# Optimization experiments

Hardware: AMD Instinct MI355X
Metric: run time of the kernel (lower is better)

Reference implementation:

```python
import jax, jax.numpy as jnp
import numpy as np
from jax import lax

K_ADA = 0.1
EPS = 1e-5
B, G = 2, 96
C0, C1, C2, C3, F = 1, 16, 32, 64, 64


def adanorm(x, g):
    # AdaNorm over the last (channel) axis: w * (1 - k*xn) * xn
    mean = x.mean(-1, keepdims=True)
    var = ((x - mean) ** 2).mean(-1, keepdims=True) + EPS
    xn = (x - mean) * lax.rsqrt(var)
    return g * (1.0 - K_ADA * xn) * xn


def conv3d(x, w, b, stride):
    # x: [B,D,H,W,Cin], w: [3,3,3,Cin,Cout], padding 1
    y = lax.conv_general_dilated(x, w, (stride,) * 3, [(1, 1)] * 3,
                                 dimension_numbers=('NDHWC', 'DHWIO', 'NDHWC'))
    return y + b


def downsample_mask(m):
    # active output sites of SparseConv3d(k=3, s=2, p=1): any active input in window
    return lax.reduce_window(m, 0.0, lax.max, (1, 3, 3, 3), (1, 2, 2, 2),
                             [(0, 0), (1, 1), (1, 1), (1, 1)])


def setup_inputs() -> dict:
    key = jax.random.key(0)
    ks = jax.random.split(key, 20)
    mask = (jax.random.uniform(ks[0], (B, G, G, G)) < 0.05).astype(jnp.float32)
    x = jax.random.normal(ks[1], (B, G, G, G, C0), jnp.float32) * mask[..., None]

    def wconv(k, cin, cout):
        return jax.random.normal(k, (3, 3, 3, cin, cout), jnp.float32) / np.sqrt(27.0 * cin)

    inp = {'x': x, 'mask': mask}
    chans = [(C0, C1), (C1, C2), (C2, C2), (C2, C3), (C3, C3)]
    for i, (ci, co) in enumerate(chans, start=1):
        inp[f'w{i}'] = wconv(ks[2 * i], ci, co)
        inp[f'b{i}'] = jax.random.normal(ks[2 * i + 1], (co,), jnp.float32) * 0.01
        inp[f'g{i}'] = jnp.ones((co,), jnp.float32)
    inp['wh'] = jax.random.normal(ks[12], (C3, F), jnp.float32) / np.sqrt(C3)
    inp['bh'] = jax.random.normal(ks[13], (F,), jnp.float32) * 0.01
    inp['gh'] = jnp.ones((F,), jnp.float32)
    return inp


def reference(x, mask, w1, b1, g1, w2, b2, g2, w3, b3, g3, w4, b4, g4, w5, b5, g5, wh, bh, gh):
    m1 = mask
    h = conv3d(x, w1, b1, 1) * m1[..., None]            # SubMConv3d
    h = jax.nn.relu(adanorm(h, g1)) * m1[..., None]
    m2 = downsample_mask(m1)
    h = conv3d(h, w2, b2, 2) * m2[..., None]            # SparseConv3d s=2
    h = jax.nn.relu(adanorm(h, g2)) * m2[..., None]
    h = conv3d(h, w3, b3, 1) * m2[..., None]            # SubMConv3d
    h = jax.nn.relu(adanorm(h, g3)) * m2[..., None]
    m3 = downsample_mask(m2)
    h = conv3d(h, w4, b4, 2) * m3[..., None]            # SparseConv3d s=2
    h = jax.nn.relu(adanorm(h, g4)) * m3[..., None]
    h = conv3d(h, w5, b5, 1) * m3[..., None]            # SubMConv3d
    h = jax.nn.relu(adanorm(h, g5)) * m3[..., None]
    # SparseGlobalMaxPool over active voxels
    neg = jnp.asarray(-3.0e38, h.dtype)
    pooled = jnp.where(m3[..., None] > 0, h, neg).max(axis=(1, 2, 3))  # [B, C3]
    # head: Linear -> AdaNorm -> ReLU -> Dropout(eval = identity)
    out = jax.nn.relu(adanorm(pooled @ wh + bh, gh))
    return out
```

## Files before the change

kernel.cpp:

```cpp
#include <hip/hip_runtime.h>
#include <math.h>

#define K_ADA 0.1f
#define NEPS 1e-5f

typedef __attribute__((ext_vector_type(8))) short short8;
typedef __attribute__((ext_vector_type(4))) float f32x4;
typedef unsigned short ushort_t;

__device__ __forceinline__ ushort_t f2b(float f) {
    union { float f; unsigned u; } v; v.f = f;
    unsigned r = (v.u + 0x7fffu + ((v.u >> 16) & 1u)) >> 16;
    return (ushort_t)r;
}

__device__ __forceinline__ float wave_sum64(float v) {
#pragma unroll
    for (int m = 1; m < 64; m <<= 1) v += __shfl_xor(v, m, 64);
    return v;
}

__host__ __device__ constexpr int tapd2(int tap) {
    return tap >= 27 ? 0 : (tap / 9) * 81 + ((tap / 3) % 3) * 9 + (tap % 3);
}

template <int CIN, int COUT>
__device__ __forceinline__ void pack_w_el(const float* __restrict__ w,
                                          ushort_t* __restrict__ wp, int t)
{
    constexpr int NKH = CIN / 32;
    constexpr int NCT = COUT / 16;
    int jj = t & 7;
    int lane = (t >> 3) & 63;
    int rest = t >> 9;
    int kh = rest % NKH;
    int rest2 = rest / NKH;
    int ct = rest2 % NCT;
    int tap = rest2 / NCT;
    int cin = kh * 32 + (lane >> 4) * 8 + jj;
    int cout = ct * 16 + (lane & 15);
    wp[t] = f2b(w[(tap * CIN + cin) * COUT + cout]);
}

__global__ __launch_bounds__(256) void prep_k(
    const float* __restrict__ w1, const float* __restrict__ w2,
    const float* __restrict__ w3, const float* __restrict__ w4,
    const float* __restrict__ w5, const float* __restrict__ m1,
    ushort_t* __restrict__ wp1, ushort_t* __restrict__ wp2,
    ushort_t* __restrict__ wp3, ushort_t* __restrict__ wp4,
    ushort_t* __restrict__ wp5, float* __restrict__ m2,
    float* __restrict__ zeropad, int* __restrict__ counters,
    float* __restrict__ pooled)
{
    int t = blockIdx.x * 256 + threadIdx.x;
    if (t < 512) {
        int jj = t & 7;
        int lane = t >> 3;
        int tap = (lane >> 4) * 8 + jj;
        int cout = lane & 15;
        wp1[t] = (tap < 27) ? f2b(w1[tap * 16 + cout]) : (ushort_t)0;
    } else if (t < 14848) {
        int u = t - 512;
        int jj = u & 7;
        int lane = (u >> 3) & 63;
        int rest = u >> 9;
        int ct = rest & 1;
        int p = rest >> 1;
        int tap = 2 * p + (lane >> 5);
        int cin = ((lane >> 4) & 1) * 8 + jj;
        int cout = ct * 16 + (lane & 15);
        wp2[u] = (tap < 27) ? f2b(w2[(tap * 16 + cin) * 32 + cout]) : (ushort_t)0;
    } else if (t < 42496) {
        pack_w_el<32, 32>(w3, wp3, t - 14848);
    } else if (t < 97792) {
        pack_w_el<32, 64>(w4, wp4, t - 42496);
    } else if (t < 208384) {
        pack_w_el<64, 64>(w5, wp5, t - 97792);
    } else if (t < 429568) {
        int v = t - 208384;
        constexpr int GO = 48, GI = 96;
        int b = v / (GO * GO * GO);
        int r = v % (GO * GO * GO);
        int d = r / (GO * GO), h = (r / GO) % GO, x = r % GO;
        float mx = 0.f;
        for (int kd = 0; kd < 3; ++kd) {
            int zd = 2 * d + kd - 1; if ((unsigned)zd >= GI) continue;
            for (int kh = 0; kh < 3; ++kh) {
                int zh = 2 * h + kh - 1; if ((unsigned)zh >= GI) continue;
                for (int kw = 0; kw < 3; ++kw) {
                    int zx = 2 * x + kw - 1; if ((unsigned)zx >= GI) continue;
                    mx = fmaxf(mx, m1[((b * GI + zd) * GI + zh) * GI + zx]);
                }
            }
        }
        m2[v] = mx;
    } else if (t < 429576) {
        zeropad[t - 429568] = 0.f;
    } else if (t < 431624) {
        counters[t - 429576] = 0;
    } else if (t < 431752) {
        pooled[t - 431624] = 0.f;
    }
}

template <int GO, int GI>
__global__ __launch_bounds__(256) void dmask_k(const float* __restrict__ mi,
                                               float* __restrict__ mo)
{
    constexpr int N = 2 * GO * GO * GO;
    int v = blockIdx.x * 256 + threadIdx.x;
    if (v >= N) return;
    int b = v / (GO * GO * GO);
    int r = v % (GO * GO * GO);
    int d = r / (GO * GO), h = (r / GO) % GO, x = r % GO;
    float mx = 0.f;
    for (int kd = 0; kd < 3; ++kd) {
        int zd = 2 * d + kd - 1; if ((unsigned)zd >= GI) continue;
        for (int kh = 0; kh < 3; ++kh) {
            int zh = 2 * h + kh - 1; if ((unsigned)zh >= GI) continue;
            for (int kw = 0; kw < 3; ++kw) {
                int zx = 2 * x + kw - 1; if ((unsigned)zx >= GI) continue;
                mx = fmaxf(mx, mi[((b * GI + zd) * GI + zh) * GI + zx]);
            }
        }
    }
    mo[v] = mx;
}

__global__ __launch_bounds__(256) void conv1_fill_k(const float* __restrict__ m1,
                                                    ushort_t* __restrict__ h1b,
                                                    int* __restrict__ list,
                                                    int* __restrict__ counters)
{
    int v = blockIdx.x * 256 + threadIdx.x;
    const short8 z = {0, 0, 0, 0, 0, 0, 0, 0};
    short8* hp = reinterpret_cast<short8*>(h1b + (size_t)v * 16);
    hp[0] = z; hp[1] = z;
    bool act = (m1[v] != 0.f);
    unsigned long long msk = __ballot(act);
    int lane = threadIdx.x & 63;
    int gwave = v >> 6;
    int p = gwave & 63;
    int base = 0;
    int cnt = __popcll(msk);
    if (lane == 0 && cnt) base = atomicAdd(&counters[p * 32], cnt);
    base = __shfl(base, 0, 64);
    if (act) {
        int pre = __popcll(msk & ((1ull << lane) - 1ull));
        list[p * 27648 + base + pre] = v;
    }
}

__global__ __launch_bounds__(256) void conv1_act_k(const float* __restrict__ x,
                                                   const int* __restrict__ list,
                                                   const int* __restrict__ counters,
                                                   const ushort_t* __restrict__ wp1,
                                                   const float* __restrict__ bias,
                                                   const float* __restrict__ gain,
                                                   const float* __restrict__ zerof,
                                                   ushort_t* __restrict__ h1b)
{
    constexpr int G = 96, G3 = G * G * G;
    int gwave = (blockIdx.x * 256 + threadIdx.x) >> 6;
    int p = gwave & 63;
    int lw = gwave >> 6;
    int nact = counters[p * 32];
    if (nact <= 0) return;
    const int* plist = list + p * 27648;
    int lane = threadIdx.x & 63;
    int m = lane & 15, q = lane >> 4;
    int nchunk = (nact + 15) >> 4;
    float bn = bias[m], gn = gain[m];
    short8 bfr = *reinterpret_cast<const short8*>(wp1 + lane * 8);

    for (int chunk = lw; chunk < nchunk; chunk += 54) {
        int idx = chunk * 16 + m;
        int vm = plist[min(idx, nact - 1)];
        int b = vm / G3;
        int rr = vm % G3;
        int dm = rr / (G * G), hm = (rr / G) % G, xm = rr % G;

        float xs[8];
#pragma unroll
        for (int j = 0; j < 8; ++j) {
            int k = q * 8 + j;
            int kd = k / 9, kh = (k / 3) % 3, kw = k % 3;
            int id = dm + kd - 1, ih = hm + kh - 1, ix = xm + kw - 1;
            bool ok = (k < 27) && ((unsigned)id < (unsigned)G) &&
                      ((unsigned)ih < (unsigned)G) && ((unsigned)ix < (unsigned)G);
            const float* xp = ok ? (x + (((size_t)b * G + id) * G + ih) * G + ix) : zerof;
            xs[j] = *xp;
        }
        ushort_t av[8];
#pragma unroll
        for (int j = 0; j < 8; ++j) av[j] = f2b(xs[j]);
        short8 a = *reinterpret_cast<short8*>(av);
        f32x4 acc = {0.f, 0.f, 0.f, 0.f};
        acc = __builtin_amdgcn_mfma_f32_16x16x32_bf16(a, bfr, acc, 0, 0, 0);

#pragma unroll
        for (int i = 0; i < 4; ++i) {
            int oidx = chunk * 16 + q * 4 + i;
            float xv = acc[i] + bn;
            float s = xv;
#pragma unroll
            for (int mk = 1; mk < 16; mk <<= 1) s += __shfl_xor(s, mk, 64);
            float mean = s * (1.f / 16.f);
            float dd = xv - mean;
            float ss = dd * dd;
#pragma unroll
            for (int mk = 1; mk < 16; mk <<= 1) ss += __shfl_xor(ss, mk, 64);
            float rs = rsqrtf(ss * (1.f / 16.f) + NEPS);
            float xn = dd * rs;
            float o = fmaxf(gn * (1.f - K_ADA * xn) * xn, 0.f);
            if (oidx < nact) {
                int w = plist[oidx];
                h1b[(size_t)w * 16 + m] = f2b(o);
            }
        }
    }
}

__global__ __launch_bounds__(256, 4) void conv2_tile_k(
    const ushort_t* __restrict__ h1b, const ushort_t* __restrict__ wp2,
    const float* __restrict__ bias, const float* __restrict__ gain,
    const float* __restrict__ m2, const ushort_t* __restrict__ zp,
    ushort_t* __restrict__ h2b)
{
    constexpr int GI = 96, G = 48;
    __shared__ __align__(16) ushort_t halo[729 * 3 * 8];

    int bid = blockIdx.x;
    int b = bid / 1728;
    int r = bid % 1728;
    int td = r / 144, th = (r / 12) % 12, tx = r % 12;
    int d0 = 4 * td, h0 = 4 * th, x0 = 4 * tx;
    int bd = 2 * d0 - 1, bh = 2 * h0 - 1, bx = 2 * x0 - 1;

    for (int c = threadIdx.x; c < 1458; c += 256) {
        int hv = c >> 1, j = c & 1;
        int gd = bd + hv / 81;
        int gh = bh + (hv / 9) % 9;
        int gx = bx + hv % 9;
        bool ok = ((unsigned)gd < (unsigned)GI) && ((unsigned)gh < (unsigned)GI) &&
                  ((unsigned)gx < (unsigned)GI);
        const ushort_t* p = ok ? (h1b + ((((size_t)b * GI + gd) * GI + gh) * GI + gx) * 16 + j * 8) : zp;
        *reinterpret_cast<short8*>(halo + ((size_t)hv * 3 + j) * 8) =
            *reinterpret_cast<const short8*>(p);
    }
    __syncthreads();

    int wv = threadIdx.x >> 6;
    int lane = threadIdx.x & 63;
    int m = lane & 15, q = lane >> 4;
    int mh = m >> 2, mx = m & 3;
    int tq = q >> 1, hq = q & 1;
    int hbase = 162 * wv + 18 * mh + 2 * mx;

    f32x4 acc0 = {0.f, 0.f, 0.f, 0.f}, acc1 = acc0;
#pragma unroll
    for (int g = 0; g < 2; ++g) {
        short8 a[7], b0[7], b1[7];
#pragma unroll
        for (int j = 0; j < 7; ++j) {
            const int p = g * 7 + j;
            int hv = hbase + (tq ? tapd2(2 * p + 1) : tapd2(2 * p));
            a[j] = *reinterpret_cast<const short8*>(halo + ((size_t)hv * 3 + hq) * 8);
            b0[j] = *reinterpret_cast<const short8*>(wp2 + ((size_t)(p * 2 + 0) * 64 + lane) * 8);
            b1[j] = *reinterpret_cast<const short8*>(wp2 + ((size_t)(p * 2 + 1) * 64 + lane) * 8);
        }
#pragma unroll
        for (int j = 0; j < 7; ++j) {
            acc0 = __builtin_amdgcn_mfma_f32_16x16x32_bf16(a[j], b0[j], acc0, 0, 0, 0);
            acc1 = __builtin_amdgcn_mfma_f32_16x16x32_bf16(a[j], b1[j], acc1, 0, 0, 0);
        }
    }

    float b0s = bias[m], b1s = bias[16 + m];
    float g0s = gain[m], g1s = gain[16 + m];
#pragma unroll
    for (int i = 0; i < 4; ++i) {
        int rr2 = q * 4 + i;
        int w = ((b * G + d0 + wv) * G + h0 + (rr2 >> 2)) * G + x0 + (rr2 & 3);
        float xv0 = acc0[i] + b0s;
        float xv1 = acc1[i] + b1s;
        float s = xv0 + xv1;
#pragma unroll
        for (int mk = 1; mk < 16; mk <<= 1) s += __shfl_xor(s, mk, 64);
        float mean = s * (1.f / 32.f);
        float dd0 = xv0 - mean, dd1 = xv1 - mean;
        float ss = dd0 * dd0 + dd1 * dd1;
#pragma unroll
        for (int mk = 1; mk < 16; mk <<= 1) ss += __shfl_xor(ss, mk, 64);
        float rs = rsqrtf(ss * (1.f / 32.f) + NEPS);
        float mv = m2[w];
        float xn0 = dd0 * rs, xn1 = dd1 * rs;
        float o0 = fmaxf(g0s * (1.f - K_ADA * xn0) * xn0, 0.f);
        float o1 = fmaxf(g1s * (1.f - K_ADA * xn1) * xn1, 0.f);
        if (mv == 0.f) { o0 = 0.f; o1 = 0.f; }
        h2b[(size_t)w * 32 + m]      = f2b(o0);
        h2b[(size_t)w * 32 + 16 + m] = f2b(o1);
    }
}

__global__ __launch_bounds__(256, 3) void conv3_tile_k(
    const ushort_t* __restrict__ h2b, const ushort_t* __restrict__ wp3,
    const float* __restrict__ bias, const float* __restrict__ gain,
    const float* __restrict__ m2, const ushort_t* __restrict__ zp,
    ushort_t* __restrict__ h3b)
{
    constexpr int G = 48;
    __shared__ __align__(16) ushort_t halo[216 * 5 * 8];
    __shared__ float nbuf[64][33];

    int bid = blockIdx.x;
    int b = bid / 1728;
    int r = bid % 1728;
    int td = r / 144, th = (r / 12) % 12, tx = r % 12;
    int d0 = 4 * td, h0 = 4 * th, x0 = 4 * tx;
    int bd = d0 - 1, bh = h0 - 1, bx = x0 - 1;

    for (int c = threadIdx.x; c < 864; c += 256) {
        int hv = c >> 2, j = c & 3;
        int gd = bd + hv / 36;
        int gh = bh + (hv / 6) % 6;
        int gx = bx + hv % 6;
        bool ok = ((unsigned)gd < (unsigned)G) && ((unsigned)gh < (unsigned)G) &&
                  ((unsigned)gx < (unsigned)G);
        const ushort_t* p = ok ? (h2b + ((((size_t)b * G + gd) * G + gh) * G + gx) * 32 + j * 8) : zp;
        *reinterpret_cast<short8*>(halo + ((size_t)hv * 5 + j) * 8) =
            *reinterpret_cast<const short8*>(p);
    }
    __syncthreads();

    int wv = threadIdx.x >> 6;
    int lane = threadIdx.x & 63;
    int m = lane & 15, q = lane >> 4;
    int mh = m >> 2, mx = m & 3;
    int ct = wv & 1;
    int sp = wv >> 1;
    int hb0 = 36 * (2 * sp) + 6 * mh + mx;
    int hb1 = hb0 + 36;

    f32x4 acc0 = {0.f, 0.f, 0.f, 0.f}, acc1 = acc0;
#pragma unroll
    for (int g = 0; g < 3; ++g) {
        short8 a0[9], a1[9], bb[9];
#pragma unroll
        for (int j = 0; j < 9; ++j) {
            const int tap = g * 9 + j;
            const int dlt = (tap / 9) * 36 + ((tap / 3) % 3) * 6 + (tap % 3);
            a0[j] = *reinterpret_cast<const short8*>(halo + ((size_t)(hb0 + dlt) * 5 + q) * 8);
            a1[j] = *reinterpret_cast<const short8*>(halo + ((size_t)(hb1 + dlt) * 5 + q) * 8);
            bb[j] = *reinterpret_cast<const short8*>(
                wp3 + ((size_t)(tap * 2 + ct) * 64 + lane) * 8);
        }
#pragma unroll
        for (int j = 0; j < 9; ++j) {
            acc0 = __builtin_amdgcn_mfma_f32_16x16x32_bf16(a0[j], bb[j], acc0, 0, 0, 0);
            acc1 = __builtin_amdgcn_mfma_f32_16x16x32_bf16(a1[j], bb[j], acc1, 0, 0, 0);
        }
    }

    float bn = bias[ct * 16 + m];
#pragma unroll
    for (int i = 0; i < 4; ++i) {
        int rr2 = q * 4 + i;
        nbuf[(2 * sp) * 16 + rr2][ct * 16 + m]     = acc0[i] + bn;
        nbuf[(2 * sp + 1) * 16 + rr2][ct * 16 + m] = acc1[i] + bn;
    }
    __syncthreads();

    int hh = lane >> 5;
    int ch = lane & 31;
    float gns = gain[ch];
    float bswap; (void)bswap;
#pragma unroll
    for (int it = 0; it < 8; ++it) {
        int vloc = wv * 16 + it * 2 + hh;
        float val = nbuf[vloc][ch];
        float s = val;
#pragma unroll
        for (int mk = 1; mk < 32; mk <<= 1) s += __shfl_xor(s, mk, 64);
        float mean = s * (1.f / 32.f);
        float dd = val - mean;
        float ss = dd * dd;
#pragma unroll
        for (int mk = 1; mk < 32; mk <<= 1) ss += __shfl_xor(ss, mk, 64);
        float rs = rsqrtf(ss * (1.f / 32.f) + NEPS);
        int slice = vloc >> 4, rr2 = vloc & 15;
        int w = ((b * G + d0 + slice) * G + h0 + (rr2 >> 2)) * G + x0 + (rr2 & 3);
        float xn = dd * rs;
        float o = fmaxf(gns * (1.f - K_ADA * xn) * xn, 0.f);
        if (m2[w] == 0.f) o = 0.f;
        h3b[(size_t)w * 32 + ch] = f2b(o);
    }
}

template <int G_IN, int CIN, int STRIDE, bool POOL>
__global__ __launch_bounds__(256, 4) void conv45_tile_k(
    const ushort_t* __restrict__ Ab, const ushort_t* __restrict__ Wp,
    const float* __restrict__ bias, const float* __restrict__ gain,
    const float* __restrict__ mask,
    ushort_t* __restrict__ outb, unsigned* __restrict__ pooled)
{
    constexpr int G = 24;
    constexpr int NKH = CIN / 32;
    constexpr int NCH = CIN / 8;
    constexpr int PADC = NCH + 1;
    constexpr int HD = STRIDE + 3;
    constexpr int HH = STRIDE + 3;
    constexpr int HX = 3 * STRIDE + 3;
    constexpr int NHV = HD * HH * HX;
    constexpr int NCHUNK = NHV * NCH;

    __shared__ __align__(16) ushort_t halo[NHV * PADC * 8];
    __shared__ float nbuf[16][65];
    __shared__ float pbuf[4][64];

    int bid = blockIdx.x;
    int b = bid / 864;
    int r = bid % 864;
    int td = r / 72, th = (r / 6) % 12, tx = r % 6;
    int d0 = 2 * td, h0 = 2 * th, x0 = 4 * tx;
    int bd = d0 * STRIDE - 1, bh = h0 * STRIDE - 1, bx = x0 * STRIDE - 1;

    for (int c = threadIdx.x; c < NCHUNK; c += 256) {
        int hv = c / NCH, j = c % NCH;
        int gd = bd + hv / (HH * HX);
        int gh = bh + (hv / HX) % HH;
        int gx = bx + hv % HX;
        short8 val = {0, 0, 0, 0, 0, 0, 0, 0};
        if ((unsigned)gd < (unsigned)G_IN && (unsigned)gh < (unsigned)G_IN &&
            (unsigned)gx < (unsigned)G_IN)
            val = *reinterpret_cast<const short8*>(
                Ab + ((((size_t)b * G_IN + gd) * G_IN + gh) * G_IN + gx) * CIN + j * 8);
        *reinterpret_cast<short8*>(halo + ((size_t)hv * PADC + j) * 8) = val;
    }
    __syncthreads();

    int ct = threadIdx.x >> 6;
    int lane = threadIdx.x & 63;
    int m = lane & 15, q = lane >> 4;
    int md = (m >> 3) & 1, mh = (m >> 2) & 1, mx = m & 3;

    f32x4 acc = {0.f, 0.f, 0.f, 0.f};
    constexpr int NT = 27 * NKH;
    constexpr int GSZ = 9;
#pragma unroll
    for (int g = 0; g < NT / GSZ; ++g) {
        short8 ab[GSZ], bb[GSZ];
#pragma unroll
        for (int j = 0; j < GSZ; ++j) {
            int it = g * GSZ + j;
            int tap = it / NKH, k2 = it % NKH;
            const int kd = tap / 9, kh = (tap / 3) % 3, kw = tap % 3;
            int hv = ((md * STRIDE + kd) * HH + (mh * STRIDE + kh)) * HX +
                     (mx * STRIDE + kw);
            ab[j] = *reinterpret_cast<const short8*>(
                halo + ((size_t)hv * PADC + k2 * 4 + q) * 8);
            bb[j] = *reinterpret_cast<const short8*>(
                Wp + (((size_t)(tap * 4 + ct) * NKH + k2) * 64 + lane) * 8);
        }
#pragma unroll
        for (int j = 0; j < GSZ; ++j)
            acc = __builtin_amdgcn_mfma_f32_16x16x32_bf16(ab[j], bb[j], acc, 0, 0, 0);
    }

    float bn = bias[ct * 16 + m];
#pragma unroll
    for (int i = 0; i < 4; ++i) nbuf[q * 4 + i][ct * 16 + m] = acc[i] + bn;
    __syncthreads();

    float gn = gain[lane];
    float wavemax = 0.f;
#pragma unroll
    for (int i = 0; i < 4; ++i) {
        int vloc = ct * 4 + i;
        int vd = d0 + ((vloc >> 3) & 1);
        int vh = h0 + ((vloc >> 2) & 1);
        int vx = x0 + (vloc & 3);
        int w = ((b * G + vd) * G + vh) * G + vx;
        float val = nbuf[vloc][lane];
        float mean = wave_sum64(val) * (1.f / 64.f);
        float dd = val - mean;
        float var = wave_sum64(dd * dd) * (1.f / 64.f) + NEPS;
        float xn = dd * rsqrtf(var);
        float o = fmaxf(gn * (1.f - K_ADA * xn) * xn, 0.f);
        if (mask[w] == 0.f) o = 0.f;
        if (POOL) wavemax = fmaxf(wavemax, o);
        else      outb[(size_t)w * 64 + lane] = f2b(o);
    }
    if (POOL) {
        pbuf[ct][lane] = wavemax;
        __syncthreads();
        if (ct == 0) {
            float v = fmaxf(fmaxf(pbuf[0][lane], pbuf[1][lane]),
                            fmaxf(pbuf[2][lane], pbuf[3][lane]));
            atomicMax(&pooled[b * 64 + lane], __float_as_uint(v));
        }
    }
}

__global__ __launch_bounds__(128) void head_k(const float* __restrict__ pooled,
                                              const float* __restrict__ wh,
                                              const float* __restrict__ bh,
                                              const float* __restrict__ gh,
                                              float* __restrict__ out)
{
    __shared__ float pl[2][64];
    int t = threadIdx.x;
    int b = t >> 6;
    int f = t & 63;
    pl[b][f] = pooled[b * 64 + f];
    __syncthreads();
    float acc = bh[f];
#pragma unroll
    for (int k = 0; k < 64; ++k) acc += pl[b][k] * wh[k * 64 + f];
    float mean = wave_sum64(acc) * (1.f / 64.f);
    float dd = acc - mean;
    float var = wave_sum64(dd * dd) * (1.f / 64.f) + NEPS;
    float xn = dd * rsqrtf(var);
    float val = gh[f] * (1.f - K_ADA * xn) * xn;
    out[t] = fmaxf(val, 0.f);
}

extern "C" void kernel_launch(void* const* d_in, const int* in_sizes, int n_in,
                              void* d_out, int out_size, void* d_ws, size_t ws_size,
                              hipStream_t stream)
{
    const float* x  = (const float*)d_in[0];
    const float* m1 = (const float*)d_in[1];
    const float* w1 = (const float*)d_in[2];
    const float* b1 = (const float*)d_in[3];
    const float* g1 = (const float*)d_in[4];
    const float* w2 = (const float*)d_in[5];
    const float* b2 = (const float*)d_in[6];
    const float* g2 = (const float*)d_in[7];
    const float* w3 = (const float*)d_in[8];
    const float* b3 = (const float*)d_in[9];
    const float* g3 = (const float*)d_in[10];
    const float* w4 = (const float*)d_in[11];
    const float* b4 = (const float*)d_in[12];
    const float* g4 = (const float*)d_in[13];
    const float* w5 = (const float*)d_in[14];
    const float* b5 = (const float*)d_in[15];
    const float* g5 = (const float*)d_in[16];
    const float* wh = (const float*)d_in[17];
    const float* bh = (const float*)d_in[18];
    const float* gh = (const float*)d_in[19];
    float* out = (float*)d_out;

    float* ws = (float*)d_ws;
    ushort_t* h1b = (ushort_t*)ws;
    ushort_t* h2b = (ushort_t*)(ws + 14155776);
    ushort_t* h3b = (ushort_t*)(ws + 17694720);
    ushort_t* h4b = (ushort_t*)(ws + 21233664);
    float* m2 = ws + 22118400;
    float* m3 = ws + 22339584;
    ushort_t* wp1 = (ushort_t*)(ws + 22367232);
    ushort_t* wp2 = (ushort_t*)(ws + 22367488);
    ushort_t* wp3 = (ushort_t*)(ws + 22374656);
    ushort_t* wp4 = (ushort_t*)(ws + 22388480);
    ushort_t* wp5 = (ushort_t*)(ws + 22416128);
    float* zeropad = ws + 22471424;
    int* counters = (int*)(ws + 22471432);
    float* pooled = ws + 22473480;
    int* list = (int*)(ws + 14155776);

    prep_k<<<1687, 256, 0, stream>>>(w1, w2, w3, w4, w5, m1,
                                     wp1, wp2, wp3, wp4, wp5, m2, zeropad,
                                     counters, pooled);
    dmask_k<24, 48><<<108, 256, 0, stream>>>(m2, m3);

    const ushort_t* zp = (const ushort_t*)zeropad;
    conv1_fill_k<<<6912, 256, 0, stream>>>(m1, h1b, list, counters);
    conv1_act_k<<<864, 256, 0, stream>>>(x, list, counters, wp1, b1, g1, zeropad, h1b);
    conv2_tile_k<<<3456, 256, 0, stream>>>(h1b, wp2, b2, g2, m2, zp, h2b);
    conv3_tile_k<<<3456, 256, 0, stream>>>(h2b, wp3, b3, g3, m2, zp, h3b);
    conv45_tile_k<48, 32, 2, false><<<1728, 256, 0, stream>>>(h3b, wp4, b4, g4, m3, h4b, nullptr);
    conv45_tile_k<24, 64, 1, true><<<1728, 256, 0, stream>>>(h4b, wp5, b5, g5, m3, nullptr,
                                                             (unsigned*)pooled);
    head_k<<<1, 128, 0, stream>>>(pooled, wh, bh, gh, out);
}
```

Baseline: 237.1 us.

## Fuse conv1 into conv2 tile kernel, recomputing conv1 on halo in LDS

Removes the separate conv1 fill/list/activation kernels and the full-resolution h1 buffer. Each conv2 tile now loads a raw input halo and mask into shared memory, computes conv1+AdaNorm for the 9x9x9 halo in LDS (skipping inactive 16-voxel groups), then runs conv2 from LDS. The m3 downsample-mask computation is folded into extra blocks of the same launch. This avoids writing and re-reading the large 96^3x16 bf16 intermediate and cuts launches, at the cost of recomputing halo overlap and extra LDS pressure.

```diff
diff --git a/kernel.cpp b/kernel.cpp
--- a/kernel.cpp
+++ b/kernel.cpp
@@ -49,8 +49,7 @@
     ushort_t* __restrict__ wp1, ushort_t* __restrict__ wp2,
     ushort_t* __restrict__ wp3, ushort_t* __restrict__ wp4,
     ushort_t* __restrict__ wp5, float* __restrict__ m2,
-    float* __restrict__ zeropad, int* __restrict__ counters,
-    float* __restrict__ pooled)
+    float* __restrict__ zeropad, float* __restrict__ pooled)
 {
     int t = blockIdx.x * 256 + threadIdx.x;
     if (t < 512) {
@@ -96,163 +95,125 @@
         m2[v] = mx;
     } else if (t < 429576) {
         zeropad[t - 429568] = 0.f;
-    } else if (t < 431624) {
-        counters[t - 429576] = 0;
-    } else if (t < 431752) {
-        pooled[t - 431624] = 0.f;
-    }
-}
-
-template <int GO, int GI>
-__global__ __launch_bounds__(256) void dmask_k(const float* __restrict__ mi,
-                                               float* __restrict__ mo)
-{
-    constexpr int N = 2 * GO * GO * GO;
-    int v = blockIdx.x * 256 + threadIdx.x;
-    if (v >= N) return;
-    int b = v / (GO * GO * GO);
-    int r = v % (GO * GO * GO);
-    int d = r / (GO * GO), h = (r / GO) % GO, x = r % GO;
-    float mx = 0.f;
-    for (int kd = 0; kd < 3; ++kd) {
-        int zd = 2 * d + kd - 1; if ((unsigned)zd >= GI) continue;
-        for (int kh = 0; kh < 3; ++kh) {
-            int zh = 2 * h + kh - 1; if ((unsigned)zh >= GI) continue;
-            for (int kw = 0; kw < 3; ++kw) {
-                int zx = 2 * x + kw - 1; if ((unsigned)zx >= GI) continue;
-                mx = fmaxf(mx, mi[((b * GI + zd) * GI + zh) * GI + zx]);
+    } else if (t < 429704) {
+        pooled[t - 429576] = 0.f;
+    }
+}
+
+__global__ __launch_bounds__(256, 3) void conv12_k(
+    const float* __restrict__ x, const float* __restrict__ m1,
+    const ushort_t* __restrict__ wp1, const float* __restrict__ b1,
+    const float* __restrict__ g1, const ushort_t* __restrict__ wp2,
+    const float* __restrict__ b2, const float* __restrict__ g2,
+    const float* __restrict__ m2, float* __restrict__ m3,
+    ushort_t* __restrict__ h2b)
+{
+    if (blockIdx.x >= 3456) {
+        int v = (blockIdx.x - 3456) * 256 + threadIdx.x;
+        constexpr int GO = 24, GI = 48;
+        int b = v / (GO * GO * GO);
+        int r = v % (GO * GO * GO);
+        int d = r / (GO * GO), h = (r / GO) % GO, xx = r % GO;
+        float mx = 0.f;
+        for (int kd = 0; kd < 3; ++kd) {
+            int zd = 2 * d + kd - 1; if ((unsigned)zd >= GI) continue;
+            for (int kh = 0; kh < 3; ++kh) {
+                int zh = 2 * h + kh - 1; if ((unsigned)zh >= GI) continue;
+                for (int kw = 0; kw < 3; ++kw) {
+                    int zx = 2 * xx + kw - 1; if ((unsigned)zx >= GI) continue;
+                    mx = fmaxf(mx, m2[((b * GI + zd) * GI + zh) * GI + zx]);
+                }
             }
         }
-    }
-    mo[v] = mx;
-}
-
-__global__ __launch_bounds__(256) void conv1_fill_k(const float* __restrict__ m1,
-                                                    ushort_t* __restrict__ h1b,
-                                                    int* __restrict__ list,
-                                                    int* __restrict__ counters)
-{
-    int v = blockIdx.x * 256 + threadIdx.x;
-    const short8 z = {0, 0, 0, 0, 0, 0, 0, 0};
-    short8* hp = reinterpret_cast<short8*>(h1b + (size_t)v * 16);
-    hp[0] = z; hp[1] = z;
-    bool act = (m1[v] != 0.f);
-    unsigned long long msk = __ballot(act);
-    int lane = threadIdx.x & 63;
-    int gwave = v >> 6;
-    int p = gwave & 63;
-    int base = 0;
-    int cnt = __popcll(msk);
-    if (lane == 0 && cnt) base = atomicAdd(&counters[p * 32], cnt);
-    base = __shfl(base, 0, 64);
-    if (act) {
-        int pre = __popcll(msk & ((1ull << lane) - 1ull));
-        list[p * 27648 + base + pre] = v;
-    }
-}
-
-__global__ __launch_bounds__(256) void conv1_act_k(const float* __restrict__ x,
-                                                   const int* __restrict__ list,
-                                                   const int* __restrict__ counters,
-                                                   const ushort_t* __restrict__ wp1,
-                                                   const float* __restrict__ bias,
-                                                   const float* __restrict__ gain,
-                                                   const float* __restrict__ zerof,
-                                                   ushort_t* __restrict__ h1b)
-{
-    constexpr int G = 96, G3 = G * G * G;
-    int gwave = (blockIdx.x * 256 + threadIdx.x) >> 6;
-    int p = gwave & 63;
-    int lw = gwave >> 6;
-    int nact = counters[p * 32];
-    if (nact <= 0) return;
-    const int* plist = list + p * 27648;
-    int lane = threadIdx.x & 63;
-    int m = lane & 15, q = lane >> 4;
-    int nchunk = (nact + 15) >> 4;
-    float bn = bias[m], gn = gain[m];
-    short8 bfr = *reinterpret_cast<const short8*>(wp1 + lane * 8);
-
-    for (int chunk = lw; chunk < nchunk; chunk += 54) {
-        int idx = chunk * 16 + m;
-        int vm = plist[min(idx, nact - 1)];
-        int b = vm / G3;
-        int rr = vm % G3;
-        int dm = rr / (G * G), hm = (rr / G) % G, xm = rr % G;
-
-        float xs[8];
-#pragma unroll
-        for (int j = 0; j < 8; ++j) {
-            int k = q * 8 + j;
-            int kd = k / 9, kh = (k / 3) % 3, kw = k % 3;
-            int id = dm + kd - 1, ih = hm + kh - 1, ix = xm + kw - 1;
-            bool ok = (k < 27) && ((unsigned)id < (unsigned)G) &&
-                      ((unsigned)ih < (unsigned)G) && ((unsigned)ix < (unsigned)G);
-            const float* xp = ok ? (x + (((size_t)b * G + id) * G + ih) * G + ix) : zerof;
-            xs[j] = *xp;
-        }
-        ushort_t av[8];
-#pragma unroll
-        for (int j = 0; j < 8; ++j) av[j] = f2b(xs[j]);
-        short8 a = *reinterpret_cast<short8*>(av);
-        f32x4 acc = {0.f, 0.f, 0.f, 0.f};
-        acc = __builtin_amdgcn_mfma_f32_16x16x32_bf16(a, bfr, acc, 0, 0, 0);
-
-#pragma unroll
-        for (int i = 0; i < 4; ++i) {
-            int oidx = chunk * 16 + q * 4 + i;
-            float xv = acc[i] + bn;
-            float s = xv;
-#pragma unroll
-            for (int mk = 1; mk < 16; mk <<= 1) s += __shfl_xor(s, mk, 64);
-            float mean = s * (1.f / 16.f);
-            float dd = xv - mean;
-            float ss = dd * dd;
-#pragma unroll
-            for (int mk = 1; mk < 16; mk <<= 1) ss += __shfl_xor(ss, mk, 64);
-            float rs = rsqrtf(ss * (1.f / 16.f) + NEPS);
-            float xn = dd * rs;
-            float o = fmaxf(gn * (1.f - K_ADA * xn) * xn, 0.f);
-            if (oidx < nact) {
-                int w = plist[oidx];
-                h1b[(size_t)w * 16 + m] = f2b(o);
-            }
-        }
-    }
-}
-
-__global__ __launch_bounds__(256, 4) void conv2_tile_k(
-    const ushort_t* __restrict__ h1b, const ushort_t* __restrict__ wp2,
-    const float* __restrict__ bias, const float* __restrict__ gain,
-    const float* __restrict__ m2, const ushort_t* __restrict__ zp,
-    ushort_t* __restrict__ h2b)
-{
-    constexpr int GI = 96, G = 48;
-    __shared__ __align__(16) ushort_t halo[729 * 3 * 8];
+        m3[v] = mx;
+        return;
+    }
+
+    constexpr int GX = 96, G = 48;
+    __shared__ float xh[1332];
+    __shared__ float m1h[729];
+    __shared__ __align__(16) ushort_t h1h[729 * 3 * 8];
 
     int bid = blockIdx.x;
     int b = bid / 1728;
     int r = bid % 1728;
     int td = r / 144, th = (r / 12) % 12, tx = r % 12;
     int d0 = 4 * td, h0 = 4 * th, x0 = 4 * tx;
-    int bd = 2 * d0 - 1, bh = 2 * h0 - 1, bx = 2 * x0 - 1;
-
-    for (int c = threadIdx.x; c < 1458; c += 256) {
-        int hv = c >> 1, j = c & 1;
-        int gd = bd + hv / 81;
-        int gh = bh + (hv / 9) % 9;
-        int gx = bx + hv % 9;
-        bool ok = ((unsigned)gd < (unsigned)GI) && ((unsigned)gh < (unsigned)GI) &&
-                  ((unsigned)gx < (unsigned)GI);
-        const ushort_t* p = ok ? (h1b + ((((size_t)b * GI + gd) * GI + gh) * GI + gx) * 16 + j * 8) : zp;
-        *reinterpret_cast<short8*>(halo + ((size_t)hv * 3 + j) * 8) =
-            *reinterpret_cast<const short8*>(p);
+    int xd = 2 * d0 - 2, xe = 2 * h0 - 2, xf = 2 * x0 - 2;
+
+    for (int c = threadIdx.x; c < 1331; c += 256) {
+        int i = c / 121, j = (c / 11) % 11, k = c % 11;
+        int gd = xd + i, gh = xe + j, gx = xf + k;
+        bool ok = ((unsigned)gd < (unsigned)GX) && ((unsigned)gh < (unsigned)GX) &&
+                  ((unsigned)gx < (unsigned)GX);
+        xh[c] = ok ? x[((size_t)(b * GX + gd) * GX + gh) * GX + gx] : 0.f;
+    }
+    if (threadIdx.x == 0) xh[1331] = 0.f;
+    for (int c = threadIdx.x; c < 729; c += 256) {
+        int i = c / 81, j = (c / 9) % 9, k = c % 9;
+        int gd = xd + 1 + i, gh = xe + 1 + j, gx = xf + 1 + k;
+        bool ok = ((unsigned)gd < (unsigned)GX) && ((unsigned)gh < (unsigned)GX) &&
+                  ((unsigned)gx < (unsigned)GX);
+        m1h[c] = ok ? m1[((size_t)(b * GX + gd) * GX + gh) * GX + gx] : 0.f;
     }
     __syncthreads();
 
     int wv = threadIdx.x >> 6;
     int lane = threadIdx.x & 63;
     int m = lane & 15, q = lane >> 4;
+
+    {
+        float bn = b1[m], gn = g1[m];
+        short8 bfr = *reinterpret_cast<const short8*>(wp1 + lane * 8);
+        for (int t = wv; t < 46; t += 4) {
+            int vt = t * 16;
+            int vm = min(vt + m, 728);
+            bool av = (vt + m < 729) && (m1h[vm] != 0.f);
+            if (__any(av)) {
+                int a = vm / 81, bb2 = (vm / 9) % 9, cc = vm % 9;
+                ushort_t avb[8];
+#pragma unroll
+                for (int j = 0; j < 8; ++j) {
+                    int k = q * 8 + j;
+                    int kd = k / 9, kh = (k / 3) % 3, kw = k % 3;
+                    int idx = (k < 27) ? ((a + kd) * 121 + (bb2 + kh) * 11 + (cc + kw))
+                                       : 1331;
+                    avb[j] = f2b(xh[idx]);
+                }
+                short8 af = *reinterpret_cast<short8*>(avb);
+                f32x4 acc = {0.f, 0.f, 0.f, 0.f};
+                acc = __builtin_amdgcn_mfma_f32_16x16x32_bf16(af, bfr, acc, 0, 0, 0);
+#pragma unroll
+                for (int i = 0; i < 4; ++i) {
+                    int vox = vt + q * 4 + i;
+                    float xv = acc[i] + bn;
+                    float s = xv;
+#pragma unroll
+                    for (int mk = 1; mk < 16; mk <<= 1) s += __shfl_xor(s, mk, 64);
+                    float mean = s * (1.f / 16.f);
+                    float dd = xv - mean;
+                    float ss = dd * dd;
+#pragma unroll
+                    for (int mk = 1; mk < 16; mk <<= 1) ss += __shfl_xor(ss, mk, 64);
+                    float rs = rsqrtf(ss * (1.f / 16.f) + NEPS);
+                    float xn = dd * rs;
+                    float o = fmaxf(gn * (1.f - K_ADA * xn) * xn, 0.f);
+                    if (vox < 729) {
+                        h1h[vox * 24 + (m >> 3) * 8 + (m & 7)] =
+                            (m1h[vox] != 0.f) ? f2b(o) : (ushort_t)0;
+                    }
+                }
+            } else {
+#pragma unroll
+                for (int i = 0; i < 4; ++i) {
+                    int vox = vt + q * 4 + i;
+                    if (vox < 729) h1h[vox * 24 + (m >> 3) * 8 + (m & 7)] = 0;
+                }
+            }
+        }
+    }
+    __syncthreads();
+
     int mh = m >> 2, mx = m & 3;
     int tq = q >> 1, hq = q & 1;
     int hbase = 162 * wv + 18 * mh + 2 * mx;
@@ -260,24 +221,24 @@
     f32x4 acc0 = {0.f, 0.f, 0.f, 0.f}, acc1 = acc0;
 #pragma unroll
     for (int g = 0; g < 2; ++g) {
-        short8 a[7], b0[7], b1[7];
+        short8 a[7], bb0[7], bb1[7];
 #pragma unroll
         for (int j = 0; j < 7; ++j) {
             const int p = g * 7 + j;
             int hv = hbase + (tq ? tapd2(2 * p + 1) : tapd2(2 * p));
-            a[j] = *reinterpret_cast<const short8*>(halo + ((size_t)hv * 3 + hq) * 8);
-            b0[j] = *reinterpret_cast<const short8*>(wp2 + ((size_t)(p * 2 + 0) * 64 + lane) * 8);
-            b1[j] = *reinterpret_cast<const short8*>(wp2 + ((size_t)(p * 2 + 1) * 64 + lane) * 8);
+            a[j] = *reinterpret_cast<const short8*>(h1h + ((size_t)hv * 3 + hq) * 8);
+            bb0[j] = *reinterpret_cast<const short8*>(wp2 + ((size_t)(p * 2 + 0) * 64 + lane) * 8);
+            bb1[j] = *reinterpret_cast<const short8*>(wp2 + ((size_t)(p * 2 + 1) * 64 + lane) * 8);
         }
 #pragma unroll
         for (int j = 0; j < 7; ++j) {
-            acc0 = __builtin_amdgcn_mfma_f32_16x16x32_bf16(a[j], b0[j], acc0, 0, 0, 0);
-            acc1 = __builtin_amdgcn_mfma_f32_16x16x32_bf16(a[j], b1[j], acc1, 0, 0, 0);
-        }
-    }
-
-    float b0s = bias[m], b1s = bias[16 + m];
-    float g0s = gain[m], g1s = gain[16 + m];
+            acc0 = __builtin_amdgcn_mfma_f32_16x16x32_bf16(a[j], bb0[j], acc0, 0, 0, 0);
+            acc1 = __builtin_amdgcn_mfma_f32_16x16x32_bf16(a[j], bb1[j], acc1, 0, 0, 0);
+        }
+    }
+
+    float b0s = b2[m], b1s = b2[16 + m];
+    float g0s = g2[m], g1s = g2[16 + m];
 #pragma unroll
     for (int i = 0; i < 4; ++i) {
         int rr2 = q * 4 + i;
@@ -374,7 +335,6 @@
     int hh = lane >> 5;
     int ch = lane & 31;
     float gns = gain[ch];
-    float bswap; (void)bswap;
 #pragma unroll
     for (int it = 0; it < 8; ++it) {
         int vloc = wv * 16 + it * 2 + hh;
@@ -552,31 +512,24 @@
     float* out = (float*)d_out;
 
     float* ws = (float*)d_ws;
-    ushort_t* h1b = (ushort_t*)ws;
-    ushort_t* h2b = (ushort_t*)(ws + 14155776);
-    ushort_t* h3b = (ushort_t*)(ws + 17694720);
-    ushort_t* h4b = (ushort_t*)(ws + 21233664);
-    float* m2 = ws + 22118400;
-    float* m3 = ws + 22339584;
-    ushort_t* wp1 = (ushort_t*)(ws + 22367232);
-    ushort_t* wp2 = (ushort_t*)(ws + 22367488);
-    ushort_t* wp3 = (ushort_t*)(ws + 22374656);
-    ushort_t* wp4 = (ushort_t*)(ws + 22388480);
-    ushort_t* wp5 = (ushort_t*)(ws + 22416128);
-    float* zeropad = ws + 22471424;
-    int* counters = (int*)(ws + 22471432);
-    float* pooled = ws + 22473480;
-    int* list = (int*)(ws + 14155776);
-
-    prep_k<<<1687, 256, 0, stream>>>(w1, w2, w3, w4, w5, m1,
-                                     wp1, wp2, wp3, wp4, wp5, m2, zeropad,
-                                     counters, pooled);
-    dmask_k<24, 48><<<108, 256, 0, stream>>>(m2, m3);
+    ushort_t* h2b = (ushort_t*)ws;
+    ushort_t* h3b = (ushort_t*)(ws + 3538944);
+    ushort_t* h4b = (ushort_t*)(ws + 7077888);
+    float* m2 = ws + 7962624;
+    float* m3 = ws + 8183808;
+    ushort_t* wp1 = (ushort_t*)(ws + 8211456);
+    ushort_t* wp2 = (ushort_t*)(ws + 8211712);
+    ushort_t* wp3 = (ushort_t*)(ws + 8218880);
+    ushort_t* wp4 = (ushort_t*)(ws + 8232704);
+    ushort_t* wp5 = (ushort_t*)(ws + 8260352);
+    float* zeropad = ws + 8315648;
+    float* pooled = ws + 8315656;
+
+    prep_k<<<1679, 256, 0, stream>>>(w1, w2, w3, w4, w5, m1,
+                                     wp1, wp2, wp3, wp4, wp5, m2, zeropad, pooled);
 
     const ushort_t* zp = (const ushort_t*)zeropad;
-    conv1_fill_k<<<6912, 256, 0, stream>>>(m1, h1b, list, counters);
-    conv1_act_k<<<864, 256, 0, stream>>>(x, list, counters, wp1, b1, g1, zeropad, h1b);
-    conv2_tile_k<<<3456, 256, 0, stream>>>(h1b, wp2, b2, g2, m2, zp, h2b);
+    conv12_k<<<3564, 256, 0, stream>>>(x, m1, wp1, b1, g1, wp2, b2, g2, m2, m3, h2b);
     conv3_tile_k<<<3456, 256, 0, stream>>>(h2b, wp3, b3, g3, m2, zp, h3b);
     conv45_tile_k<48, 32, 2, false><<<1728, 256, 0, stream>>>(h3b, wp4, b4, g4, m3, h4b, nullptr);
     conv45_tile_k<24, 64, 1, true><<<1728, 256, 0, stream>>>(h4b, wp5, b5, g5, m3, nullptr,
```

After: 293.6 us. 1.24x slower.
